# Kernel optimization log

Hardware: AMD Instinct MI355X
Metric: run time of the kernel (lower is better)

Reference implementation:

```python
import jax, jax.numpy as jnp
import numpy as np

N_NODES = 50000
N_EDGES = 800000
IN_DIM = 128
HID = 64
NUM_GRAPHS = 64


def _gcn_conv(x, W, b, src, dst, num_nodes):
    """PyG GCNConv: out = D^-1/2 (A+I) D^-1/2 (x W) + b, messages scattered to dst."""
    h = x @ W  # [N, out]
    ones = jnp.ones((src.shape[0],), dtype=x.dtype)
    # degree at target nodes, self-loop adds 1
    deg = jax.ops.segment_sum(ones, dst, num_segments=num_nodes) + 1.0
    dinv = jax.lax.rsqrt(deg)  # [N]
    norm = dinv[src] * dinv[dst]  # [E]
    msgs = h[src] * norm[:, None]  # [E, out] gather-scale
    agg = jax.ops.segment_sum(msgs, dst, num_segments=num_nodes)  # scatter-add
    # self-loop contribution: norm_ii = dinv[i]^2
    agg = agg + h * (dinv * dinv)[:, None]
    return agg + b


def setup_inputs() -> dict:
    key = jax.random.key(0)
    k = jax.random.split(key, 10)
    x = jax.random.normal(k[0], (N_NODES, IN_DIM), dtype=jnp.float32)
    edge_index = jax.random.randint(k[1], (2, N_EDGES), 0, N_NODES, dtype=jnp.int32)
    batch = jnp.sort(jax.random.randint(k[2], (N_NODES,), 0, NUM_GRAPHS, dtype=jnp.int32))
    # Glorot-ish params
    W1 = jax.random.normal(k[3], (IN_DIM, HID), dtype=jnp.float32) / np.sqrt(IN_DIM)
    b1 = jnp.zeros((HID,), dtype=jnp.float32)
    W2 = jax.random.normal(k[4], (HID, HID), dtype=jnp.float32) / np.sqrt(HID)
    b2 = jnp.zeros((HID,), dtype=jnp.float32)
    Wlin = jax.random.normal(k[5], (HID, 1), dtype=jnp.float32) / np.sqrt(HID)
    blin = jnp.zeros((1,), dtype=jnp.float32)
    return {"x": x, "edge_index": edge_index, "batch": batch,
            "W1": W1, "b1": b1, "W2": W2, "b2": b2, "Wlin": Wlin, "blin": blin}


def reference(x, edge_index, batch, W1, b1, W2, b2, Wlin, blin):
    src, dst = edge_index[0], edge_index[1]
    h = _gcn_conv(x, W1, b1, src, dst, N_NODES)
    h = jax.nn.relu(h)  # dropout is identity in eval mode
    h = _gcn_conv(h, W2, b2, src, dst, N_NODES)
    h = jax.nn.relu(h)
    # global mean pool per graph
    sums = jax.ops.segment_sum(h, batch, num_segments=NUM_GRAPHS)  # [G, HID]
    cnts = jax.ops.segment_sum(jnp.ones((N_NODES,), h.dtype), batch, num_segments=NUM_GRAPHS)
    pooled = sums / jnp.maximum(cnts, 1.0)[:, None]
    return pooled @ Wlin + blin  # [G, 1]
```

## Files before the change

### kernel.cpp

```cpp
#include <hip/hip_runtime.h>
#include <hip/hip_fp16.h>

#define N_NODES 50000
#define N_EDGES 800000
#define IN_DIM 128
#define HID 64
#define NUM_GRAPHS 64
#define NB 196
#define NBLK 64

__device__ inline float4 load_h4(const __half* p) {
    const __half2* q = (const __half2*)p;
    float2 a = __half22float2(q[0]);
    float2 b = __half22float2(q[1]);
    return make_float4(a.x, a.y, b.x, b.y);
}
__device__ inline void store_h4(__half* p, float4 v) {
    __half2* q = (__half2*)p;
    q[0] = __floats2half2_rn(v.x, v.y);
    q[1] = __floats2half2_rn(v.z, v.w);
}
__device__ inline void load_h8(const __half* p, float* f) {
    float4 r = *(const float4*)p;
    const __half2* h = (const __half2*)&r;
    float2 a0 = __half22float2(h[0]);
    float2 a1 = __half22float2(h[1]);
    float2 a2 = __half22float2(h[2]);
    float2 a3 = __half22float2(h[3]);
    f[0] = a0.x; f[1] = a0.y; f[2] = a1.x; f[3] = a1.y;
    f[4] = a2.x; f[5] = a2.y; f[6] = a3.x; f[7] = a3.y;
}
__device__ inline void store_h8(__half* p, const float* f) {
    __half2 hs[4];
    hs[0] = __floats2half2_rn(f[0], f[1]);
    hs[1] = __floats2half2_rn(f[2], f[3]);
    hs[2] = __floats2half2_rn(f[4], f[5]);
    hs[3] = __floats2half2_rn(f[6], f[7]);
    *(float4*)p = *(const float4*)hs;
}

template <int K, typename TIN, bool SCALE>
__device__ __forceinline__ void gemm_body(const TIN* __restrict__ A, const float* __restrict__ W,
                                          const float* __restrict__ dinv, __half* __restrict__ out,
                                          int nRows, int node0, float* xs, float* ws) {
    int tid = threadIdx.x;
    int c0 = (tid & 15) * 4, n0 = (tid >> 4) * 4;
    float acc[4][4] = {};
    for (int kb = 0; kb < K; kb += 64) {
        for (int i = tid; i < 64 * 16; i += 256) {
            int k = i >> 4, c4 = (i & 15) * 4;
            *(float4*)&ws[k * 68 + c4] = *(const float4*)&W[(size_t)(kb + k) * 64 + c4];
        }
        for (int i = tid; i < 64 * 16; i += 256) {
            int n = i >> 4, k4 = (i & 15) * 4;
            int gn = node0 + n;
            float4 v;
            if (gn < nRows) {
                if constexpr (sizeof(TIN) == 4) v = *(const float4*)&A[(size_t)gn * K + kb + k4];
                else                            v = load_h4((const __half*)&A[(size_t)gn * K + kb + k4]);
            } else v = make_float4(0.f, 0.f, 0.f, 0.f);
            *(float4*)&xs[n * 68 + k4] = v;
        }
        __syncthreads();
        for (int k = 0; k < 64; k += 4) {
            float4 x0 = *(const float4*)&xs[(n0 + 0) * 68 + k];
            float4 x1 = *(const float4*)&xs[(n0 + 1) * 68 + k];
            float4 x2 = *(const float4*)&xs[(n0 + 2) * 68 + k];
            float4 x3 = *(const float4*)&xs[(n0 + 3) * 68 + k];
            #define KSTEP(KK, F) { \
                float4 wr = *(const float4*)&ws[(k + KK) * 68 + c0]; \
                acc[0][0] += x0.F * wr.x; acc[0][1] += x0.F * wr.y; acc[0][2] += x0.F * wr.z; acc[0][3] += x0.F * wr.w; \
                acc[1][0] += x1.F * wr.x; acc[1][1] += x1.F * wr.y; acc[1][2] += x1.F * wr.z; acc[1][3] += x1.F * wr.w; \
                acc[2][0] += x2.F * wr.x; acc[2][1] += x2.F * wr.y; acc[2][2] += x2.F * wr.z; acc[2][3] += x2.F * wr.w; \
                acc[3][0] += x3.F * wr.x; acc[3][1] += x3.F * wr.y; acc[3][2] += x3.F * wr.z; acc[3][3] += x3.F * wr.w; }
            KSTEP(0, x)
            KSTEP(1, y)
            KSTEP(2, z)
            KSTEP(3, w)
            #undef KSTEP
        }
        __syncthreads();
    }
    #pragma unroll
    for (int i = 0; i < 4; i++) {
        int gn = node0 + n0 + i;
        if (gn < nRows) {
            float sc = 1.0f;
            if constexpr (SCALE) sc = dinv[gn];
            store_h4(&out[(size_t)gn * 64 + c0],
                     make_float4(acc[i][0] * sc, acc[i][1] * sc, acc[i][2] * sc, acc[i][3] * sc));
        }
    }
}

__global__ __launch_bounds__(256) void k1_kernel(const int* __restrict__ dst, int* __restrict__ hist_g,
                                                 const float* __restrict__ x, const float* __restrict__ W1,
                                                 __half* __restrict__ h1) {
    __shared__ __align__(16) float smem[2 * 64 * 68];
    int blk = blockIdx.x, tid = threadIdx.x;
    if (blk < NBLK) {
        int* h = (int*)smem;
        for (int i = tid; i < NB; i += 256) h[i] = 0;
        __syncthreads();
        const int NI = N_EDGES / 4;
        for (int i = blk * 256 + tid; i < NI; i += NBLK * 256) {
            int4 d = ((const int4*)dst)[i];
            atomicAdd(&h[d.x >> 8], 1);
            atomicAdd(&h[d.y >> 8], 1);
            atomicAdd(&h[d.z >> 8], 1);
            atomicAdd(&h[d.w >> 8], 1);
        }
        __syncthreads();
        for (int i = tid; i < NB; i += 256) hist_g[i * NBLK + blk] = h[i];
    } else {
        int node0 = (blk - NBLK) * 64;
        gemm_body<IN_DIM, float, false>(x, W1, nullptr, h1, N_NODES, node0, smem, smem + 64 * 68);
    }
}

__global__ __launch_bounds__(256) void k2_binscan(const int* __restrict__ hist_g,
                                                  const int* __restrict__ src, const int* __restrict__ dst,
                                                  int* __restrict__ binned, int* __restrict__ bstart,
                                                  int* __restrict__ offs) {
    __shared__ int ld[NB * NBLK];
    __shared__ int cur[NB];
    __shared__ int wsum[4];
    int tid = threadIdx.x, blk = blockIdx.x;
    for (int i = tid; i < NB * NBLK; i += 256) ld[i] = hist_g[i];
    __syncthreads();
    const int CH = (NB * NBLK) / 256;
    int base = tid * CH;
    int s = 0;
    for (int k = 0; k < CH; k++) { int v = ld[base + k]; ld[base + k] = s; s += v; }
    int lane = tid & 63, wid = tid >> 6;
    int inc = s;
    #pragma unroll
    for (int d = 1; d < 64; d <<= 1) { int t = __shfl_up(inc, d, 64); if (lane >= d) inc += t; }
    if (lane == 63) wsum[wid] = inc;
    __syncthreads();
    if (tid == 0) {
        int a = 0;
        for (int w = 0; w < 4; w++) { int t = wsum[w]; wsum[w] = a; a += t; }
    }
    __syncthreads();
    int off = wsum[wid] + inc - s;
    for (int k = 0; k < CH; k++) ld[base + k] += off;
    __syncthreads();
    for (int b = tid; b < NB; b += 256) cur[b] = ld[b * NBLK + blk];
    if (blk == 0) {
        for (int b = tid; b < NB; b += 256) bstart[b] = ld[b * NBLK];
        if (tid == 0) { bstart[NB] = N_EDGES; offs[N_NODES] = N_EDGES; }
    }
    __syncthreads();
    const int NI = N_EDGES / 4;
    for (int i = blk * 256 + tid; i < NI; i += NBLK * 256) {
        int4 sv = ((const int4*)src)[i];
        int4 dv = ((const int4*)dst)[i];
        int p0 = atomicAdd(&cur[dv.x >> 8], 1); binned[p0] = (sv.x & 0xFFFF) | ((dv.x & 255) << 16);
        int p1 = atomicAdd(&cur[dv.y >> 8], 1); binned[p1] = (sv.y & 0xFFFF) | ((dv.y & 255) << 16);
        int p2 = atomicAdd(&cur[dv.z >> 8], 1); binned[p2] = (sv.z & 0xFFFF) | ((dv.z & 255) << 16);
        int p3 = atomicAdd(&cur[dv.w >> 8], 1); binned[p3] = (sv.w & 0xFFFF) | ((dv.w & 255) << 16);
    }
}

__global__ __launch_bounds__(256) void build_kernel(const int* __restrict__ binned, const int* __restrict__ bstart,
                                                    int* __restrict__ offs, float* __restrict__ dinv,
                                                    unsigned short* __restrict__ csr_src) {
    __shared__ int cnt[256];
    __shared__ int excl[256];
    __shared__ int rnk[256];
    __shared__ int wtot[4];
    int b = blockIdx.x, tid = threadIdx.x;
    int base = bstart[b];
    int end  = bstart[b + 1];
    cnt[tid] = 0; rnk[tid] = 0;
    __syncthreads();
    for (int j = base + tid; j < end; j += 256) atomicAdd(&cnt[(binned[j] >> 16) & 255], 1);
    __syncthreads();
    int v = cnt[tid];
    int lane = tid & 63, wid = tid >> 6;
    int inc = v;
    #pragma unroll
    for (int d = 1; d < 64; d <<= 1) { int t = __shfl_up(inc, d, 64); if (lane >= d) inc += t; }
    if (lane == 63) wtot[wid] = inc;
    __syncthreads();
    if (tid == 0) {
        int a = 0;
        for (int w = 0; w < 4; w++) { int t = wtot[w]; wtot[w] = a; a += t; }
    }
    __syncthreads();
    excl[tid] = wtot[wid] + inc - v;
    int node = b * 256 + tid;
    if (node < N_NODES) {
        offs[node] = base + excl[tid];
        dinv[node] = rsqrtf((float)v + 1.0f);
    }
    __syncthreads();
    for (int j = base + tid; j < end; j += 256) {
        int e = binned[j];
        int l = (e >> 16) & 255;
        int r = atomicAdd(&rnk[l], 1);
        csr_src[base + excl[l] + r] = (unsigned short)(e & 0xFFFF);
    }
}

__global__ __launch_bounds__(256) void agg1f_kernel(const __half* __restrict__ hd, const int* __restrict__ offs,
                                                    const unsigned short* __restrict__ csr_src,
                                                    const float* __restrict__ dinv, const float* __restrict__ bias,
                                                    const float* __restrict__ W2,
                                                    __half* __restrict__ out) {
    int lane = threadIdx.x & 63;
    int node = blockIdx.x * 4 + (threadIdx.x >> 6);
    int g = lane >> 3;
    int cc = (lane & 7) * 8;
    float acc[8] = {};
    int beg = offs[node], end = offs[node + 1];
    #pragma unroll 2
    for (int j = beg + g; j < end; j += 8) {
        int s = csr_src[j];
        float dv = dinv[s];
        float hv[8];
        load_h8(&hd[(size_t)s * 64 + cc], hv);
        #pragma unroll
        for (int i = 0; i < 8; i++) acc[i] = fmaf(hv[i], dv, acc[i]);
    }
    #pragma unroll
    for (int m = 8; m <= 32; m <<= 1) {
        #pragma unroll
        for (int i = 0; i < 8; i++) acc[i] += __shfl_xor(acc[i], m, 64);
    }
    float di = dinv[node];
    float d2 = di * di;
    float hn[8];
    load_h8(&hd[(size_t)node * 64 + cc], hn);
    float4 bv0 = *(const float4*)&bias[cc];
    float4 bv1 = *(const float4*)&bias[cc + 4];
    float bb[8] = {bv0.x, bv0.y, bv0.z, bv0.w, bv1.x, bv1.y, bv1.z, bv1.w};
    float r[8];
    #pragma unroll
    for (int i = 0; i < 8; i++) r[i] = fmaxf(fmaf(di, acc[i], fmaf(d2, hn[i], bb[i])), 0.0f);
    float dsum = 0.0f;
    #pragma unroll
    for (int c = 0; c < 64; c++) {
        float a = __shfl(r[c & 7], c >> 3, 64);
        dsum = fmaf(a, W2[c * 64 + lane], dsum);
    }
    out[(size_t)node * 64 + lane] = __float2half(di * dsum);
}

__global__ __launch_bounds__(256) void agg2dot_kernel(const __half* __restrict__ hd, const int* __restrict__ offs,
                                                      const unsigned short* __restrict__ csr_src,
                                                      const float* __restrict__ dinv, const float* __restrict__ bias,
                                                      const float* __restrict__ Wlin,
                                                      float* __restrict__ ndot) {
    int lane = threadIdx.x & 63;
    int node = blockIdx.x * 4 + (threadIdx.x >> 6);
    int g = lane >> 3;
    int cc = (lane & 7) * 8;
    float acc[8] = {};
    int beg = offs[node], end = offs[node + 1];
    #pragma unroll 2
    for (int j = beg + g; j < end; j += 8) {
        int s = csr_src[j];
        float hv[8];
        load_h8(&hd[(size_t)s * 64 + cc], hv);
        #pragma unroll
        for (int i = 0; i < 8; i++) acc[i] += hv[i];
    }
    #pragma unroll
    for (int m = 8; m <= 32; m <<= 1) {
        #pragma unroll
        for (int i = 0; i < 8; i++) acc[i] += __shfl_xor(acc[i], m, 64);
    }
    if (g == 0) {
        float di = dinv[node];
        float hn[8];
        load_h8(&hd[(size_t)node * 64 + cc], hn);
        float4 bv0 = *(const float4*)&bias[cc];
        float4 bv1 = *(const float4*)&bias[cc + 4];
        float bb[8] = {bv0.x, bv0.y, bv0.z, bv0.w, bv1.x, bv1.y, bv1.z, bv1.w};
        float4 wl0 = *(const float4*)&Wlin[cc];
        float4 wl1 = *(const float4*)&Wlin[cc + 4];
        float ww[8] = {wl0.x, wl0.y, wl0.z, wl0.w, wl1.x, wl1.y, wl1.z, wl1.w};
        float d = 0.0f;
        #pragma unroll
        for (int i = 0; i < 8; i++) {
            float rr = fmaxf(fmaf(di, acc[i] + hn[i], bb[i]), 0.0f);
            d = fmaf(rr, ww[i], d);
        }
        #pragma unroll
        for (int m = 1; m < 8; m <<= 1) d += __shfl_xor(d, m, 64);
        if ((lane & 7) == 0) ndot[node] = d;
    }
}

__global__ __launch_bounds__(256) void graphred_kernel(const float* __restrict__ ndot, const int* __restrict__ batch,
                                                       const float* __restrict__ blin, float* __restrict__ out) {
    __shared__ float wpart[4];
    int g = blockIdx.x;
    int tid = threadIdx.x;
    int lo = 0, hi = N_NODES;
    while (lo < hi) { int m = (lo + hi) >> 1; if (batch[m] < g) lo = m + 1; else hi = m; }
    int lo2 = lo, hi2 = N_NODES;
    while (lo2 < hi2) { int m = (lo2 + hi2) >> 1; if (batch[m] < g + 1) lo2 = m + 1; else hi2 = m; }
    float s = 0.0f;
    for (int i = lo + tid; i < lo2; i += 256) s += ndot[i];
    int lane = tid & 63, wid = tid >> 6;
    #pragma unroll
    for (int m = 32; m > 0; m >>= 1) s += __shfl_down(s, m, 64);
    if (lane == 0) wpart[wid] = s;
    __syncthreads();
    if (tid == 0) {
        float t = wpart[0] + wpart[1] + wpart[2] + wpart[3];
        float cnt = (float)(lo2 - lo);
        out[g] = t / fmaxf(cnt, 1.0f) + blin[0];
    }
}

extern "C" void kernel_launch(void* const* d_in, const int* in_sizes, int n_in,
                              void* d_out, int out_size, void* d_ws, size_t ws_size,
                              hipStream_t stream) {
    const float* x    = (const float*)d_in[0];
    const int*   ei   = (const int*)d_in[1];
    const int*   batch= (const int*)d_in[2];
    const float* W1   = (const float*)d_in[3];
    const float* b1   = (const float*)d_in[4];
    const float* W2   = (const float*)d_in[5];
    const float* b2   = (const float*)d_in[6];
    const float* Wlin = (const float*)d_in[7];
    const float* blin = (const float*)d_in[8];
    float* out = (float*)d_out;
    const int* srcA = ei;
    const int* dstA = ei + N_EDGES;

    char* p = (char*)d_ws;
    auto alloc = [&](size_t n) { char* r = p; p += (n + 255) & ~(size_t)255; return r; };
    int*    hist_g  = (int*)alloc((size_t)NB * NBLK * 4);
    int*    bstart  = (int*)alloc((size_t)(NB + 1) * 4);
    int*    offs    = (int*)alloc((size_t)(N_NODES + 1) * 4);
    int*    binned  = (int*)alloc((size_t)N_EDGES * 4);
    unsigned short* csr_src = (unsigned short*)alloc((size_t)N_EDGES * 2);
    float*  dinv    = (float*)alloc((size_t)N_NODES * 4);
    float*  ndot    = (float*)alloc((size_t)N_NODES * 4);
    __half* bufA    = (__half*)alloc((size_t)N_NODES * 64 * 2);
    __half* bufB    = (__half*)alloc((size_t)N_NODES * 64 * 2);

    const int GEMM1_BLOCKS = (N_NODES + 63) / 64;
    k1_kernel<<<NBLK + GEMM1_BLOCKS, 256, 0, stream>>>(dstA, hist_g, x, W1, bufA);
    k2_binscan<<<NBLK, 256, 0, stream>>>(hist_g, srcA, dstA, binned, bstart, offs);
    build_kernel<<<NB, 256, 0, stream>>>(binned, bstart, offs, dinv, csr_src);
    agg1f_kernel<<<N_NODES / 4, 256, 0, stream>>>(bufA, offs, csr_src, dinv, b1, W2, bufB);
    agg2dot_kernel<<<N_NODES / 4, 256, 0, stream>>>(bufB, offs, csr_src, dinv, b2, Wlin, ndot);
    graphred_kernel<<<NUM_GRAPHS, 256, 0, stream>>>(ndot, batch, blin, out);
}
```

Baseline: 210.5 us.

## Split feature columns into halves for cache-resident gathers and separate layer-2 GEMM

Node feature tensors are stored as two 32-column fp16 halves, and each aggregation runs twice, once per half, so the gathered table (about 3.2 MB) is more likely to stay in cache during random neighbour gathers. The W2 transform that was fused into the first aggregation via shuffles moves into a separate tiled GEMM kernel. The second aggregation writes two partial dot vectors that the graph reduction sums. The trade-off is more kernel launches, the CSR index and offset arrays being read twice, and an extra full pass over activations for the standalone GEMM.

```diff
diff --git a/kernel.cpp b/kernel.cpp
--- a/kernel.cpp
+++ b/kernel.cpp
@@ -39,9 +39,11 @@
     *(float4*)p = *(const float4*)hs;
 }
 
-template <int K, typename TIN, bool SCALE>
-__device__ __forceinline__ void gemm_body(const TIN* __restrict__ A, const float* __restrict__ W,
-                                          const float* __restrict__ dinv, __half* __restrict__ out,
+template <int K, bool IN_SPLIT, bool SCALE>
+__device__ __forceinline__ void gemm_body(const float* __restrict__ Af,
+                                          const __half* __restrict__ Alo, const __half* __restrict__ Ahi,
+                                          const float* __restrict__ W, const float* __restrict__ dinv,
+                                          __half* __restrict__ out_lo, __half* __restrict__ out_hi,
                                           int nRows, int node0, float* xs, float* ws) {
     int tid = threadIdx.x;
     int c0 = (tid & 15) * 4, n0 = (tid >> 4) * 4;
@@ -56,8 +58,13 @@
             int gn = node0 + n;
             float4 v;
             if (gn < nRows) {
-                if constexpr (sizeof(TIN) == 4) v = *(const float4*)&A[(size_t)gn * K + kb + k4];
-                else                            v = load_h4((const __half*)&A[(size_t)gn * K + kb + k4]);
+                if constexpr (!IN_SPLIT) {
+                    v = *(const float4*)&Af[(size_t)gn * K + kb + k4];
+                } else {
+                    int k = kb + k4;
+                    v = (k < 32) ? load_h4(&Alo[(size_t)gn * 32 + k])
+                                 : load_h4(&Ahi[(size_t)gn * 32 + (k - 32)]);
+                }
             } else v = make_float4(0.f, 0.f, 0.f, 0.f);
             *(float4*)&xs[n * 68 + k4] = v;
         }
@@ -87,15 +94,16 @@
         if (gn < nRows) {
             float sc = 1.0f;
             if constexpr (SCALE) sc = dinv[gn];
-            store_h4(&out[(size_t)gn * 64 + c0],
-                     make_float4(acc[i][0] * sc, acc[i][1] * sc, acc[i][2] * sc, acc[i][3] * sc));
+            float4 r = make_float4(acc[i][0] * sc, acc[i][1] * sc, acc[i][2] * sc, acc[i][3] * sc);
+            if (c0 < 32) store_h4(&out_lo[(size_t)gn * 32 + c0], r);
+            else         store_h4(&out_hi[(size_t)gn * 32 + (c0 - 32)], r);
         }
     }
 }
 
 __global__ __launch_bounds__(256) void k1_kernel(const int* __restrict__ dst, int* __restrict__ hist_g,
                                                  const float* __restrict__ x, const float* __restrict__ W1,
-                                                 __half* __restrict__ h1) {
+                                                 __half* __restrict__ h1_lo, __half* __restrict__ h1_hi) {
     __shared__ __align__(16) float smem[2 * 64 * 68];
     int blk = blockIdx.x, tid = threadIdx.x;
     if (blk < NBLK) {
@@ -114,7 +122,8 @@
         for (int i = tid; i < NB; i += 256) hist_g[i * NBLK + blk] = h[i];
     } else {
         int node0 = (blk - NBLK) * 64;
-        gemm_body<IN_DIM, float, false>(x, W1, nullptr, h1, N_NODES, node0, smem, smem + 64 * 68);
+        gemm_body<IN_DIM, false, false>(x, nullptr, nullptr, W1, nullptr, h1_lo, h1_hi,
+                                        N_NODES, node0, smem, smem + 64 * 68);
     }
 }
 
@@ -204,83 +213,86 @@
     }
 }
 
-__global__ __launch_bounds__(256) void agg1f_kernel(const __half* __restrict__ hd, const int* __restrict__ offs,
+__global__ __launch_bounds__(256) void agg1h_kernel(const __half* __restrict__ hd32, const int* __restrict__ offs,
                                                     const unsigned short* __restrict__ csr_src,
-                                                    const float* __restrict__ dinv, const float* __restrict__ bias,
-                                                    const float* __restrict__ W2,
-                                                    __half* __restrict__ out) {
+                                                    const float* __restrict__ dinv, const float* __restrict__ bias32,
+                                                    __half* __restrict__ out32) {
     int lane = threadIdx.x & 63;
     int node = blockIdx.x * 4 + (threadIdx.x >> 6);
-    int g = lane >> 3;
-    int cc = (lane & 7) * 8;
+    int grp = lane >> 2;
+    int cc = (lane & 3) * 8;
     float acc[8] = {};
     int beg = offs[node], end = offs[node + 1];
     #pragma unroll 2
-    for (int j = beg + g; j < end; j += 8) {
+    for (int j = beg + grp; j < end; j += 16) {
         int s = csr_src[j];
         float dv = dinv[s];
         float hv[8];
-        load_h8(&hd[(size_t)s * 64 + cc], hv);
+        load_h8(&hd32[(size_t)s * 32 + cc], hv);
         #pragma unroll
         for (int i = 0; i < 8; i++) acc[i] = fmaf(hv[i], dv, acc[i]);
     }
     #pragma unroll
-    for (int m = 8; m <= 32; m <<= 1) {
+    for (int m = 4; m <= 32; m <<= 1) {
         #pragma unroll
         for (int i = 0; i < 8; i++) acc[i] += __shfl_xor(acc[i], m, 64);
     }
-    float di = dinv[node];
-    float d2 = di * di;
-    float hn[8];
-    load_h8(&hd[(size_t)node * 64 + cc], hn);
-    float4 bv0 = *(const float4*)&bias[cc];
-    float4 bv1 = *(const float4*)&bias[cc + 4];
-    float bb[8] = {bv0.x, bv0.y, bv0.z, bv0.w, bv1.x, bv1.y, bv1.z, bv1.w};
-    float r[8];
-    #pragma unroll
-    for (int i = 0; i < 8; i++) r[i] = fmaxf(fmaf(di, acc[i], fmaf(d2, hn[i], bb[i])), 0.0f);
-    float dsum = 0.0f;
-    #pragma unroll
-    for (int c = 0; c < 64; c++) {
-        float a = __shfl(r[c & 7], c >> 3, 64);
-        dsum = fmaf(a, W2[c * 64 + lane], dsum);
-    }
-    out[(size_t)node * 64 + lane] = __float2half(di * dsum);
-}
-
-__global__ __launch_bounds__(256) void agg2dot_kernel(const __half* __restrict__ hd, const int* __restrict__ offs,
-                                                      const unsigned short* __restrict__ csr_src,
-                                                      const float* __restrict__ dinv, const float* __restrict__ bias,
-                                                      const float* __restrict__ Wlin,
-                                                      float* __restrict__ ndot) {
+    if (grp == 0) {
+        float di = dinv[node];
+        float d2 = di * di;
+        float hn[8];
+        load_h8(&hd32[(size_t)node * 32 + cc], hn);
+        float4 bv0 = *(const float4*)&bias32[cc];
+        float4 bv1 = *(const float4*)&bias32[cc + 4];
+        float bb[8] = {bv0.x, bv0.y, bv0.z, bv0.w, bv1.x, bv1.y, bv1.z, bv1.w};
+        float r[8];
+        #pragma unroll
+        for (int i = 0; i < 8; i++) r[i] = fmaxf(fmaf(di, acc[i], fmaf(d2, hn[i], bb[i])), 0.0f);
+        store_h8(&out32[(size_t)node * 32 + cc], r);
+    }
+}
+
+__global__ __launch_bounds__(256) void gemm2_kernel(const __half* __restrict__ Alo, const __half* __restrict__ Ahi,
+                                                    const float* __restrict__ W, const float* __restrict__ dinv,
+                                                    __half* __restrict__ out_lo, __half* __restrict__ out_hi) {
+    __shared__ __align__(16) float smem[2 * 64 * 68];
+    gemm_body<HID, true, true>(nullptr, Alo, Ahi, W, dinv, out_lo, out_hi,
+                               N_NODES, blockIdx.x * 64, smem, smem + 64 * 68);
+}
+
+__global__ __launch_bounds__(256) void agg2h_kernel(const __half* __restrict__ hd32, const int* __restrict__ offs,
+                                                    const unsigned short* __restrict__ csr_src,
+                                                    const float* __restrict__ dinv, const float* __restrict__ bias32,
+                                                    const float* __restrict__ wlin32,
+                                                    float* __restrict__ nd) {
     int lane = threadIdx.x & 63;
     int node = blockIdx.x * 4 + (threadIdx.x >> 6);
-    int g = lane >> 3;
-    int cc = (lane & 7) * 8;
+    int grp = lane >> 2;
+    int cc = (lane & 3) * 8;
     float acc[8] = {};
     int beg = offs[node], end = offs[node + 1];
     #pragma unroll 2
-    for (int j = beg + g; j < end; j += 8) {
+    for (int j = beg + grp; j < end; j += 16) {
         int s = csr_src[j];
         float hv[8];
-        load_h8(&hd[(size_t)s * 64 + cc], hv);
+        load_h8(&hd32[(size_t)s * 32 + cc], hv);
         #pragma unroll
         for (int i = 0; i < 8; i++) acc[i] += hv[i];
     }
     #pragma unroll
-    for (int m = 8; m <= 32; m <<= 1) {
+    for (int m = 4; m <= 32; m <<= 1) {
         #pragma unroll
         for (int i = 0; i < 8; i++) acc[i] += __shfl_xor(acc[i], m, 64);
     }
-    if (g == 0) {
+    if (grp == 0) {
         float di = dinv[node];
         float hn[8];
-        load_h8(&hd[(size_t)node * 64 + cc], hn);
-        float4 bv0 = *(const float4*)&bias[cc];
-        float4 bv1 = *(const float4*)&bias[cc + 4];
+        load_h8(&hd32[(size_t)node * 32 + cc], hn);
+        float4 bv0 = *(const float4*)&bias32[cc];
+        float4 bv1 = *(const float4*)&bias32[cc + 4];
         float bb[8] = {bv0.x, bv0.y, bv0.z, bv0.w, bv1.x, bv1.y, bv1.z, bv1.w};
-        float4 wl0 = *(const float4*)&Wlin[cc];
-        float4 wl1 = *(const float4*)&Wlin[cc + 4];
+        float4 wl0 = *(const float4*)&wlin32[cc];
+        float4 wl1 = *(const float4*)&wlin32[cc + 4];
         float ww[8] = {wl0.x, wl0.y, wl0.z, wl0.w, wl1.x, wl1.y, wl1.z, wl1.w};
         float d = 0.0f;
         #pragma unroll
@@ -288,13 +300,14 @@
             float rr = fmaxf(fmaf(di, acc[i] + hn[i], bb[i]), 0.0f);
             d = fmaf(rr, ww[i], d);
         }
-        #pragma unroll
-        for (int m = 1; m < 8; m <<= 1) d += __shfl_xor(d, m, 64);
-        if ((lane & 7) == 0) ndot[node] = d;
-    }
-}
-
-__global__ __launch_bounds__(256) void graphred_kernel(const float* __restrict__ ndot, const int* __restrict__ batch,
+        d += __shfl_xor(d, 1, 64);
+        d += __shfl_xor(d, 2, 64);
+        if ((lane & 3) == 0) nd[node] = d;
+    }
+}
+
+__global__ __launch_bounds__(256) void graphred_kernel(const float* __restrict__ ndA, const float* __restrict__ ndB,
+                                                       const int* __restrict__ batch,
                                                        const float* __restrict__ blin, float* __restrict__ out) {
     __shared__ float wpart[4];
     int g = blockIdx.x;
@@ -304,7 +317,7 @@
     int lo2 = lo, hi2 = N_NODES;
     while (lo2 < hi2) { int m = (lo2 + hi2) >> 1; if (batch[m] < g + 1) lo2 = m + 1; else hi2 = m; }
     float s = 0.0f;
-    for (int i = lo + tid; i < lo2; i += 256) s += ndot[i];
+    for (int i = lo + tid; i < lo2; i += 256) s += ndA[i] + ndB[i];
     int lane = tid & 63, wid = tid >> 6;
     #pragma unroll
     for (int m = 32; m > 0; m >>= 1) s += __shfl_down(s, m, 64);
@@ -341,15 +354,23 @@
     int*    binned  = (int*)alloc((size_t)N_EDGES * 4);
     unsigned short* csr_src = (unsigned short*)alloc((size_t)N_EDGES * 2);
     float*  dinv    = (float*)alloc((size_t)N_NODES * 4);
-    float*  ndot    = (float*)alloc((size_t)N_NODES * 4);
-    __half* bufA    = (__half*)alloc((size_t)N_NODES * 64 * 2);
-    __half* bufB    = (__half*)alloc((size_t)N_NODES * 64 * 2);
+    float*  ndotA   = (float*)alloc((size_t)N_NODES * 4);
+    float*  ndotB   = (float*)alloc((size_t)N_NODES * 4);
+    __half* h1_lo   = (__half*)alloc((size_t)N_NODES * 32 * 2);
+    __half* h1_hi   = (__half*)alloc((size_t)N_NODES * 32 * 2);
+    __half* act_lo  = (__half*)alloc((size_t)N_NODES * 32 * 2);
+    __half* act_hi  = (__half*)alloc((size_t)N_NODES * 32 * 2);
+    __half* h2_lo   = (__half*)alloc((size_t)N_NODES * 32 * 2);
+    __half* h2_hi   = (__half*)alloc((size_t)N_NODES * 32 * 2);
 
     const int GEMM1_BLOCKS = (N_NODES + 63) / 64;
-    k1_kernel<<<NBLK + GEMM1_BLOCKS, 256, 0, stream>>>(dstA, hist_g, x, W1, bufA);
+    k1_kernel<<<NBLK + GEMM1_BLOCKS, 256, 0, stream>>>(dstA, hist_g, x, W1, h1_lo, h1_hi);
     k2_binscan<<<NBLK, 256, 0, stream>>>(hist_g, srcA, dstA, binned, bstart, offs);
     build_kernel<<<NB, 256, 0, stream>>>(binned, bstart, offs, dinv, csr_src);
-    agg1f_kernel<<<N_NODES / 4, 256, 0, stream>>>(bufA, offs, csr_src, dinv, b1, W2, bufB);
-    agg2dot_kernel<<<N_NODES / 4, 256, 0, stream>>>(bufB, offs, csr_src, dinv, b2, Wlin, ndot);
-    graphred_kernel<<<NUM_GRAPHS, 256, 0, stream>>>(ndot, batch, blin, out);
-}
+    agg1h_kernel<<<N_NODES / 4, 256, 0, stream>>>(h1_lo, offs, csr_src, dinv, b1,      act_lo);
+    agg1h_kernel<<<N_NODES / 4, 256, 0, stream>>>(h1_hi, offs, csr_src, dinv, b1 + 32, act_hi);
+    gemm2_kernel<<<GEMM1_BLOCKS, 256, 0, stream>>>(act_lo, act_hi, W2, dinv, h2_lo, h2_hi);
+    agg2h_kernel<<<N_NODES / 4, 256, 0, stream>>>(h2_lo, offs, csr_src, dinv, b2,      Wlin,      ndotA);
+    agg2h_kernel<<<N_NODES / 4, 256, 0, stream>>>(h2_hi, offs, csr_src, dinv, b2 + 32, Wlin + 32, ndotB);
+    graphred_kernel<<<NUM_GRAPHS, 256, 0, stream>>>(ndotA, ndotB, batch, blin, out);
+}
```

After: 236.8 us. 1.13x slower.
